# Kernel tuning notes

Measured on AMD Instinct MI355X. Metric: run time of the kernel, lower is better.

Reference implementation:

```python
import jax, jax.numpy as jnp
import numpy as np

LAYERS = [3, 256, 256, 256, 256, 2]
N = 32768  # collocation points


def setup_inputs() -> dict:
    key = jax.random.key(0)
    ks = jax.random.split(key, 2 * len(LAYERS))
    inp = {"inputs": jax.random.uniform(ks[0], (N, LAYERS[0]), dtype=jnp.float32)}
    for l in range(len(LAYERS) - 1):
        std = np.sqrt(2.0 / (LAYERS[l] + LAYERS[l + 1])).astype(np.float32)
        inp[f"W{l}"] = std * jax.random.truncated_normal(
            ks[l + 1], -2.0, 2.0, (LAYERS[l], LAYERS[l + 1]), dtype=jnp.float32)
        inp[f"b{l}"] = jnp.zeros((LAYERS[l + 1],), dtype=jnp.float32)
    inp["lb"] = jnp.zeros((LAYERS[0],), dtype=jnp.float32)
    inp["ub"] = jnp.ones((LAYERS[0],), dtype=jnp.float32)
    return inp


def _net(x, Ws, bs, lb, ub):
    # normalize inputs to [-1, 1], then tanh MLP with linear final layer
    H = 2.0 * (x - lb) / (ub - lb) - 1.0
    for W, b in zip(Ws[:-1], bs[:-1]):
        H = jnp.tanh(H @ W + b)
    return H @ Ws[-1] + bs[-1]


def reference(inputs, W0, b0, W1, b1, W2, b2, W3, b3, W4, b4, lb, ub):
    Ws = [W0, W1, W2, W3, W4]
    bs = [b0, b1, b2, b3, b4]
    out = _net(inputs, Ws, bs, lb, ub)  # [N, Dout]

    f1 = lambda x: _net(x, Ws, bs, lb, ub)  # single sample [D1] -> [Dout]
    # partials_1[i][n, k] = d y_i[n] / d x[n, k]  (tf.gradients of sum over batch)
    jac = jax.vmap(jax.jacrev(f1))(inputs)  # [N, Dout, D1]
    # tf.gradients(partials_1[i], X) = grad of sum over (n, j) of dy_i/dx_j,
    # per sample: partials_2[i][n, k] = sum_j d^2 y_i[n] / (dx_j dx_k)
    g = lambda x: jax.jacrev(f1)(x).sum(axis=-1)  # [Dout]
    hess = jax.vmap(jax.jacrev(g))(inputs)  # [N, Dout, D1]

    partials_1 = jnp.transpose(jac, (1, 0, 2))   # [Dout, N, D1]
    partials_2 = jnp.transpose(hess, (1, 0, 2))  # [Dout, N, D1]
    return out, partials_1, partials_2
```

## Files before the change

kernel.cpp:

```cpp
#include <hip/hip_runtime.h>
#include <math.h>

typedef _Float16 f16x8 __attribute__((ext_vector_type(8)));
typedef _Float16 f16x4 __attribute__((ext_vector_type(4)));
typedef float    f32x4 __attribute__((ext_vector_type(4)));
typedef f16x8 f16x8_a __attribute__((may_alias));
typedef f16x4 f16x4_a __attribute__((may_alias));
typedef f32x4 f32x4_a __attribute__((may_alias));

#define MSAMP 8

__device__ __forceinline__ float tanh_fast(float x) {
    const float e = __expf(2.0f * x);
    return 1.0f - 2.0f * __builtin_amdgcn_rcpf(e + 1.0f);
}

__global__ void prep_w(const float* __restrict__ W1, const float* __restrict__ W2,
                       const float* __restrict__ W3, _Float16* __restrict__ wsw) {
    const int tid = blockIdx.x * 256 + threadIdx.x;
    if (tid >= 3 * 8 * 16 * 64 * 8) return;
    const int j    = tid & 7;
    const int lane = (tid >> 3) & 63;
    const int nt   = (tid >> 9) & 15;
    const int kt   = (tid >> 13) & 7;
    const int l    = tid >> 16;
    const float* W = (l == 0) ? W1 : (l == 1) ? W2 : W3;
    const int k = kt * 32 + (lane >> 4) * 8 + j;
    const int n = nt * 16 + (lane & 15);
    wsw[((size_t)((l * 8 + kt) * 16 + nt)) * 512 + lane * 8 + j] = (_Float16)W[k * 256 + n];
}

__global__ __launch_bounds__(256, 3)
void pinn_mfma(const float* __restrict__ X,
               const float* __restrict__ W0, const float* __restrict__ b0,
               const float* __restrict__ b1, const float* __restrict__ b2,
               const float* __restrict__ b3,
               const float* __restrict__ W4, const float* __restrict__ b4,
               const float* __restrict__ lb, const float* __restrict__ ub,
               const _Float16* __restrict__ wsw,
               float* __restrict__ out, int N)
{
    __shared__ __attribute__((aligned(16))) char  smem[32768];
    __shared__ __attribute__((aligned(16))) float redw[448];
    f16x8_a*  BV  = (f16x8_a*)smem;
    _Float16* zbh = (_Float16*)smem;

    const int t    = threadIdx.x;
    const int s0   = blockIdx.x * MSAMP;
    const int wv   = t >> 6, lane = t & 63;
    const int q    = lane >> 4, c = lane & 15;
    const int jgl  = lane >> 3, m = lane & 7;
    const int jg   = wv * 8 + jgl;
    const int kt0  = jg >> 2, lq0 = jg & 3;

    const int vidz0 = ((t >> 5) * 4 + 3) * 64 + ((t >> 3) & 3) * 16 + 8 + (t & 7);
    const int vidzw = (((wv * 2 + (lane >> 5)) * 4 + 3) * 64) + (((lane >> 3) & 3) * 16) + 8 + (lane & 7);
    const f16x8 zvec = {};

    float lbv[3], cv[3];
    #pragma unroll
    for (int k = 0; k < 3; ++k) { lbv[k] = lb[k]; cv[k] = 2.0f / (ub[k] - lbv[k]); }

    {
        const int jg0 = t >> 3, m0 = t & 7;
        const int n = s0 + m0;
        float x0 = 0.f, x1 = 0.f, x2 = 0.f;
        if (n < N) { x0 = X[n*3+0]; x1 = X[n*3+1]; x2 = X[n*3+2]; }
        const float h0 = cv[0]*(x0 - lbv[0]) - 1.0f;
        const float h1 = cv[1]*(x1 - lbv[1]) - 1.0f;
        const float h2 = cv[2]*(x2 - lbv[2]) - 1.0f;

        float w0v[8], w1v[8], w2v[8], bv[8];
        *(f32x4*)&w0v[0] = *(const f32x4*)&W0[0*256 + jg0*8];
        *(f32x4*)&w0v[4] = *(const f32x4*)&W0[0*256 + jg0*8 + 4];
        *(f32x4*)&w1v[0] = *(const f32x4*)&W0[1*256 + jg0*8];
        *(f32x4*)&w1v[4] = *(const f32x4*)&W0[1*256 + jg0*8 + 4];
        *(f32x4*)&w2v[0] = *(const f32x4*)&W0[2*256 + jg0*8];
        *(f32x4*)&w2v[4] = *(const f32x4*)&W0[2*256 + jg0*8 + 4];
        *(f32x4*)&bv[0]  = *(const f32x4*)&b0[jg0*8];
        *(f32x4*)&bv[4]  = *(const f32x4*)&b0[jg0*8 + 4];

        float st[7][8];
        #pragma unroll
        for (int jj = 0; jj < 8; ++jj) {
            const float zH  = h0*w0v[jj] + h1*w1v[jj] + h2*w2v[jj] + bv[jj];
            const float zt0 = cv[0]*w0v[jj];
            const float zt1 = cv[1]*w1v[jj];
            const float zt2 = cv[2]*w2v[jj];
            const float h   = tanh_fast(zH);
            const float dd  = 1.0f - h*h;
            const float qq  = -2.0f * h * (zt0 + zt1 + zt2);
            st[0][jj] = h;
            st[1][jj] = dd * zt0; st[2][jj] = dd * zt1; st[3][jj] = dd * zt2;
            st[4][jj] = dd * (qq*zt0); st[5][jj] = dd * (qq*zt1); st[6][jj] = dd * (qq*zt2);
        }
        const int k0a = jg0 >> 2, l0a = jg0 & 3;
        #pragma unroll
        for (int s = 0; s < 7; ++s) {
            const int r = s*8 + m0;
            const int vid = (k0a*4 + (r>>4))*64 + l0a*16 + (r & 15);
            f16x8 vh;
            #pragma unroll
            for (int jj = 0; jj < 8; ++jj) vh[jj] = (_Float16)st[s][jj];
            BV[vid] = vh;
        }
        BV[vidz0] = zvec;
    }
    __syncthreads();

    #pragma unroll 1
    for (int l = 0; l < 3; ++l) {
        const _Float16* __restrict__ Wb = wsw + (size_t)l * 65536;
        const int ktbase = 2*wv + 2;

        f32x4 acc[4][4];
        #pragma unroll
        for (int a = 0; a < 4; ++a)
            #pragma unroll
            for (int b = 0; b < 4; ++b) acc[a][b] = (f32x4){0.f, 0.f, 0.f, 0.f};

        #pragma unroll
        for (int i = 0; i < 8; ++i) {
            if (i == 6) __syncthreads();
            const int kt = (ktbase + i) & 7;
            f16x8 sh[4], wh[4];
            #pragma unroll
            for (int rt = 0; rt < 4; ++rt)
                sh[rt] = BV[(kt*4 + rt)*64 + lane];
            #pragma unroll
            for (int mtj = 0; mtj < 4; ++mtj)
                wh[mtj] = *(const f16x8*)&Wb[(size_t)(kt*16 + wv*4 + mtj)*512 + lane*8];
            #pragma unroll
            for (int mtj = 0; mtj < 4; ++mtj)
                #pragma unroll
                for (int rt = 0; rt < 4; ++rt)
                    acc[mtj][rt] = __builtin_amdgcn_mfma_f32_16x16x32_f16(wh[mtj], sh[rt],
                                                                          acc[mtj][rt], 0, 0, 0);
        }

        #pragma unroll
        for (int mtj = 0; mtj < 4; ++mtj) {
            const int jl = mtj*16 + q*4;
            #pragma unroll
            for (int rt = 0; rt < 4; ++rt) {
                const int r = rt*16 + c;
                const int h = wv*4096 + r*64 + ((jl + 4*(r&15)) & 63);
                f16x4 v;
                #pragma unroll
                for (int e = 0; e < 4; ++e) v[e] = (_Float16)acc[mtj][rt][e];
                *(f16x4_a*)&zbh[h] = v;
            }
        }
        asm volatile("s_waitcnt lgkmcnt(0)" ::: "memory");

        {
            const float* __restrict__ bb = (l == 0) ? b1 : (l == 1) ? b2 : b3;
            float bvv[8];
            *(f32x4*)&bvv[0] = *(const f32x4*)&bb[jg*8];
            *(f32x4*)&bvv[4] = *(const f32x4*)&bb[jg*8 + 4];

            float z[7][8];
            #pragma unroll
            for (int s = 0; s < 7; ++s) {
                const int r    = s*8 + m;
                const int base = wv*4096 + r*64;
                const int rot  = 4*(r & 15);
                const f16x4 a = *(const f16x4_a*)&zbh[base + ((jgl*8     + rot) & 63)];
                const f16x4 b = *(const f16x4_a*)&zbh[base + ((jgl*8 + 4 + rot) & 63)];
                #pragma unroll
                for (int e = 0; e < 4; ++e) { z[s][e] = (float)a[e]; z[s][4+e] = (float)b[e]; }
            }
            float stt[7][8];
            #pragma unroll
            for (int jj = 0; jj < 8; ++jj) {
                const float zH  = z[0][jj] + bvv[jj];
                const float zt0 = z[1][jj], zt1 = z[2][jj], zt2 = z[3][jj];
                const float zr0 = z[4][jj], zr1 = z[5][jj], zr2 = z[6][jj];
                const float h   = tanh_fast(zH);
                const float dd  = 1.0f - h*h;
                const float qq  = -2.0f * h * (zt0 + zt1 + zt2);
                stt[0][jj] = h;
                stt[1][jj] = dd * zt0; stt[2][jj] = dd * zt1; stt[3][jj] = dd * zt2;
                stt[4][jj] = dd * (zr0 + qq*zt0);
                stt[5][jj] = dd * (zr1 + qq*zt1);
                stt[6][jj] = dd * (zr2 + qq*zt2);
            }

            if (l < 2) {
                #pragma unroll
                for (int s = 0; s < 7; ++s) {
                    const int r = s*8 + m;
                    const int vid = (kt0*4 + (r>>4))*64 + lq0*16 + (r & 15);
                    f16x8 vh;
                    #pragma unroll
                    for (int jj = 0; jj < 8; ++jj) vh[jj] = (_Float16)stt[s][jj];
                    BV[vid] = vh;
                }
                BV[vidzw] = zvec;
                __syncthreads();
            } else {
                float w4r[16];
                #pragma unroll
                for (int q4 = 0; q4 < 4; ++q4)
                    *(f32x4*)&w4r[q4*4] = *(const f32x4*)&W4[jg*16 + q4*4];
                float p[2][7];
                #pragma unroll
                for (int s = 0; s < 7; ++s) {
                    float p0 = 0.f, p1 = 0.f;
                    #pragma unroll
                    for (int jj = 0; jj < 8; ++jj) {
                        p0 += stt[s][jj] * w4r[jj*2 + 0];
                        p1 += stt[s][jj] * w4r[jj*2 + 1];
                    }
                    p[0][s] = p0; p[1][s] = p1;
                }
                #pragma unroll
                for (int ch = 0; ch < 2; ++ch) {
                    #pragma unroll
                    for (int s = 0; s < 7; ++s) {
                        float v = p[ch][s];
                        v += __shfl_xor(v, 8);
                        v += __shfl_xor(v, 16);
                        v += __shfl_xor(v, 32);
                        p[ch][s] = v;
                    }
                }
                if (jgl == 0) {
                    #pragma unroll
                    for (int ch = 0; ch < 2; ++ch)
                        #pragma unroll
                        for (int s = 0; s < 7; ++s)
                            redw[(ch*56 + s*8 + m)*4 + wv] = p[ch][s];
                }
                __syncthreads();
            }
        }
    }

    if (t < 112) {
        const f32x4 vv = *(const f32x4*)&redw[t*4];
        const float v = vv[0] + vv[1] + vv[2] + vv[3];
        const int ch = t / 56, rem = t % 56, s = rem >> 3, mm = rem & 7;
        const int n = s0 + mm;
        if (n < N) {
            const size_t N2 = (size_t)N * 2, N3 = (size_t)N * 3;
            if (s == 0)      out[(size_t)n*2 + ch] = v + b4[ch];
            else if (s <= 3) out[N2 + (size_t)ch*N3 + (size_t)n*3 + (s-1)] = v;
            else             out[N2 + 2*N3 + (size_t)ch*N3 + (size_t)n*3 + (s-4)] = v;
        }
    }
}

extern "C" void kernel_launch(void* const* d_in, const int* in_sizes, int n_in,
                              void* d_out, int out_size, void* d_ws, size_t ws_size,
                              hipStream_t stream) {
    const float* X  = (const float*)d_in[0];
    const float* W0 = (const float*)d_in[1];
    const float* b0 = (const float*)d_in[2];
    const float* W1 = (const float*)d_in[3];
    const float* b1 = (const float*)d_in[4];
    const float* W2 = (const float*)d_in[5];
    const float* b2 = (const float*)d_in[6];
    const float* W3 = (const float*)d_in[7];
    const float* b3 = (const float*)d_in[8];
    const float* W4 = (const float*)d_in[9];
    const float* b4 = (const float*)d_in[10];
    const float* lb = (const float*)d_in[11];
    const float* ub = (const float*)d_in[12];
    float* out = (float*)d_out;
    _Float16* wsw = (_Float16*)d_ws;

    const int N = in_sizes[0] / 3;

    prep_w<<<768, 256, 0, stream>>>(W1, W2, W3, wsw);

    const int grid = (N + MSAMP - 1) / MSAMP;
    pinn_mfma<<<grid, 256, 0, stream>>>(X, W0, b0, b1, b2, b3, W4, b4, lb, ub,
                                        wsw, out, N);
}
```

Before: 192.5 us.

## Split each block's work across eight waves and pack activation math in fp16

Doubles the block to 512 threads so each wave owns 32 output features (2 MFMA column tiles) instead of 64, halving per-wave accumulators and spreading the MFMA and tanh work over more waves. The per-layer tangent and second-derivative propagation now runs in packed fp16 (f16x2 ops) with pkrtz conversions, and the LDS staging layout, swizzle and reduction buffer are adjusted to match. The aim is more parallelism and lower register pressure per wave at the cost of extra barrier participants and reduced precision in the derivative chain.

New measurement: 202.2 us. 5.0% more time.

```diff
diff --git a/kernel.cpp b/kernel.cpp
--- a/kernel.cpp
+++ b/kernel.cpp
@@ -3,6 +3,7 @@
 
 typedef _Float16 f16x8 __attribute__((ext_vector_type(8)));
 typedef _Float16 f16x4 __attribute__((ext_vector_type(4)));
+typedef _Float16 f16x2 __attribute__((ext_vector_type(2)));
 typedef float    f32x4 __attribute__((ext_vector_type(4)));
 typedef f16x8 f16x8_a __attribute__((may_alias));
 typedef f16x4 f16x4_a __attribute__((may_alias));
@@ -13,6 +14,16 @@
 __device__ __forceinline__ float tanh_fast(float x) {
     const float e = __expf(2.0f * x);
     return 1.0f - 2.0f * __builtin_amdgcn_rcpf(e + 1.0f);
+}
+
+__device__ __forceinline__ f16x2 pkrtz(float a, float b) {
+    return __builtin_bit_cast(f16x2, __builtin_amdgcn_cvt_pkrtz(a, b));
+}
+__device__ __forceinline__ f16x4 cat2(f16x2 a, f16x2 b) {
+    return __builtin_shufflevector(a, b, 0, 1, 2, 3);
+}
+__device__ __forceinline__ f16x4 pack4(const float* v) {
+    return cat2(pkrtz(v[0], v[1]), pkrtz(v[2], v[3]));
 }
 
 __global__ void prep_w(const float* __restrict__ W1, const float* __restrict__ W2,
@@ -30,7 +41,7 @@
     wsw[((size_t)((l * 8 + kt) * 16 + nt)) * 512 + lane * 8 + j] = (_Float16)W[k * 256 + n];
 }
 
-__global__ __launch_bounds__(256, 3)
+__global__ __launch_bounds__(512, 4)
 void pinn_mfma(const float* __restrict__ X,
                const float* __restrict__ W0, const float* __restrict__ b0,
                const float* __restrict__ b1, const float* __restrict__ b2,
@@ -41,28 +52,23 @@
                float* __restrict__ out, int N)
 {
     __shared__ __attribute__((aligned(16))) char  smem[32768];
-    __shared__ __attribute__((aligned(16))) float redw[448];
-    f16x8_a*  BV  = (f16x8_a*)smem;
-    _Float16* zbh = (_Float16*)smem;
+    __shared__ __attribute__((aligned(16))) float redw[896];
+    f16x8_a*  BV = (f16x8_a*)smem;
+    _Float16* Bh = (_Float16*)smem;
 
     const int t    = threadIdx.x;
     const int s0   = blockIdx.x * MSAMP;
     const int wv   = t >> 6, lane = t & 63;
     const int q    = lane >> 4, c = lane & 15;
-    const int jgl  = lane >> 3, m = lane & 7;
-    const int jg   = wv * 8 + jgl;
-    const int kt0  = jg >> 2, lq0 = jg & 3;
-
-    const int vidz0 = ((t >> 5) * 4 + 3) * 64 + ((t >> 3) & 3) * 16 + 8 + (t & 7);
-    const int vidzw = (((wv * 2 + (lane >> 5)) * 4 + 3) * 64) + (((lane >> 3) & 3) * 16) + 8 + (lane & 7);
-    const f16x8 zvec = {};
+    const int qd   = lane >> 3, m = lane & 7;
+    const f16x8 zvec8 = {};
 
     float lbv[3], cv[3];
     #pragma unroll
     for (int k = 0; k < 3; ++k) { lbv[k] = lb[k]; cv[k] = 2.0f / (ub[k] - lbv[k]); }
 
     {
-        const int jg0 = t >> 3, m0 = t & 7;
+        const int qd4 = t >> 3, m0 = t & 7;
         const int n = s0 + m0;
         float x0 = 0.f, x1 = 0.f, x2 = 0.f;
         if (n < N) { x0 = X[n*3+0]; x1 = X[n*3+1]; x2 = X[n*3+2]; }
@@ -70,19 +76,15 @@
         const float h1 = cv[1]*(x1 - lbv[1]) - 1.0f;
         const float h2 = cv[2]*(x2 - lbv[2]) - 1.0f;
 
-        float w0v[8], w1v[8], w2v[8], bv[8];
-        *(f32x4*)&w0v[0] = *(const f32x4*)&W0[0*256 + jg0*8];
-        *(f32x4*)&w0v[4] = *(const f32x4*)&W0[0*256 + jg0*8 + 4];
-        *(f32x4*)&w1v[0] = *(const f32x4*)&W0[1*256 + jg0*8];
-        *(f32x4*)&w1v[4] = *(const f32x4*)&W0[1*256 + jg0*8 + 4];
-        *(f32x4*)&w2v[0] = *(const f32x4*)&W0[2*256 + jg0*8];
-        *(f32x4*)&w2v[4] = *(const f32x4*)&W0[2*256 + jg0*8 + 4];
-        *(f32x4*)&bv[0]  = *(const f32x4*)&b0[jg0*8];
-        *(f32x4*)&bv[4]  = *(const f32x4*)&b0[jg0*8 + 4];
-
-        float st[7][8];
-        #pragma unroll
-        for (int jj = 0; jj < 8; ++jj) {
+        float w0v[4], w1v[4], w2v[4], bv[4];
+        *(f32x4*)w0v = *(const f32x4*)&W0[0*256 + qd4*4];
+        *(f32x4*)w1v = *(const f32x4*)&W0[1*256 + qd4*4];
+        *(f32x4*)w2v = *(const f32x4*)&W0[2*256 + qd4*4];
+        *(f32x4*)bv  = *(const f32x4*)&b0[qd4*4];
+
+        float st[7][4];
+        #pragma unroll
+        for (int jj = 0; jj < 4; ++jj) {
             const float zH  = h0*w0v[jj] + h1*w1v[jj] + h2*w2v[jj] + bv[jj];
             const float zt0 = cv[0]*w0v[jj];
             const float zt1 = cv[1]*w1v[jj];
@@ -94,44 +96,42 @@
             st[1][jj] = dd * zt0; st[2][jj] = dd * zt1; st[3][jj] = dd * zt2;
             st[4][jj] = dd * (qq*zt0); st[5][jj] = dd * (qq*zt1); st[6][jj] = dd * (qq*zt2);
         }
-        const int k0a = jg0 >> 2, l0a = jg0 & 3;
         #pragma unroll
         for (int s = 0; s < 7; ++s) {
             const int r = s*8 + m0;
-            const int vid = (k0a*4 + (r>>4))*64 + l0a*16 + (r & 15);
-            f16x8 vh;
-            #pragma unroll
-            for (int jj = 0; jj < 8; ++jj) vh[jj] = (_Float16)st[s][jj];
-            BV[vid] = vh;
-        }
-        BV[vidz0] = zvec;
+            const int vid = ((qd4>>3)*4 + (r>>4))*64 + ((qd4>>1)&3)*16 + (r & 15);
+            *(f16x4_a*)&Bh[vid*8 + (qd4&1)*4] = pack4(&st[s][0]);
+        }
+    }
+    if (t < 256) {
+        const int vid = ((t>>5)*4 + 3)*64 + ((t>>3)&3)*16 + 8 + (t&7);
+        BV[vid] = zvec8;
     }
     __syncthreads();
 
     #pragma unroll 1
     for (int l = 0; l < 3; ++l) {
         const _Float16* __restrict__ Wb = wsw + (size_t)l * 65536;
-        const int ktbase = 2*wv + 2;
-
-        f32x4 acc[4][4];
-        #pragma unroll
-        for (int a = 0; a < 4; ++a)
+
+        f32x4 acc[2][4];
+        #pragma unroll
+        for (int a = 0; a < 2; ++a)
             #pragma unroll
             for (int b = 0; b < 4; ++b) acc[a][b] = (f32x4){0.f, 0.f, 0.f, 0.f};
 
         #pragma unroll
         for (int i = 0; i < 8; ++i) {
-            if (i == 6) __syncthreads();
-            const int kt = (ktbase + i) & 7;
-            f16x8 sh[4], wh[4];
+            if (i == 7) __syncthreads();
+            const int kt = (wv + 1 + i) & 7;
+            f16x8 sh[4], wh[2];
             #pragma unroll
             for (int rt = 0; rt < 4; ++rt)
                 sh[rt] = BV[(kt*4 + rt)*64 + lane];
             #pragma unroll
-            for (int mtj = 0; mtj < 4; ++mtj)
-                wh[mtj] = *(const f16x8*)&Wb[(size_t)(kt*16 + wv*4 + mtj)*512 + lane*8];
-            #pragma unroll
-            for (int mtj = 0; mtj < 4; ++mtj)
+            for (int mtj = 0; mtj < 2; ++mtj)
+                wh[mtj] = *(const f16x8*)&Wb[(size_t)(kt*16 + wv*2 + mtj)*512 + lane*8];
+            #pragma unroll
+            for (int mtj = 0; mtj < 2; ++mtj)
                 #pragma unroll
                 for (int rt = 0; rt < 4; ++rt)
                     acc[mtj][rt] = __builtin_amdgcn_mfma_f32_16x16x32_f16(wh[mtj], sh[rt],
@@ -139,78 +139,93 @@
         }
 
         #pragma unroll
-        for (int mtj = 0; mtj < 4; ++mtj) {
+        for (int mtj = 0; mtj < 2; ++mtj) {
             const int jl = mtj*16 + q*4;
             #pragma unroll
             for (int rt = 0; rt < 4; ++rt) {
                 const int r = rt*16 + c;
-                const int h = wv*4096 + r*64 + ((jl + 4*(r&15)) & 63);
-                f16x4 v;
-                #pragma unroll
-                for (int e = 0; e < 4; ++e) v[e] = (_Float16)acc[mtj][rt][e];
-                *(f16x4_a*)&zbh[h] = v;
+                const int h = wv*2048 + r*32 + ((jl + 4*(r&7)) & 31);
+                *(f16x4_a*)&Bh[h] = cat2(pkrtz(acc[mtj][rt][0], acc[mtj][rt][1]),
+                                         pkrtz(acc[mtj][rt][2], acc[mtj][rt][3]));
             }
         }
         asm volatile("s_waitcnt lgkmcnt(0)" ::: "memory");
 
         {
             const float* __restrict__ bb = (l == 0) ? b1 : (l == 1) ? b2 : b3;
-            float bvv[8];
-            *(f32x4*)&bvv[0] = *(const f32x4*)&bb[jg*8];
-            *(f32x4*)&bvv[4] = *(const f32x4*)&bb[jg*8 + 4];
-
-            float z[7][8];
-            #pragma unroll
-            for (int s = 0; s < 7; ++s) {
-                const int r    = s*8 + m;
-                const int base = wv*4096 + r*64;
-                const int rot  = 4*(r & 15);
-                const f16x4 a = *(const f16x4_a*)&zbh[base + ((jgl*8     + rot) & 63)];
-                const f16x4 b = *(const f16x4_a*)&zbh[base + ((jgl*8 + 4 + rot) & 63)];
-                #pragma unroll
-                for (int e = 0; e < 4; ++e) { z[s][e] = (float)a[e]; z[s][4+e] = (float)b[e]; }
-            }
-            float stt[7][8];
-            #pragma unroll
-            for (int jj = 0; jj < 8; ++jj) {
-                const float zH  = z[0][jj] + bvv[jj];
-                const float zt0 = z[1][jj], zt1 = z[2][jj], zt2 = z[3][jj];
-                const float zr0 = z[4][jj], zr1 = z[5][jj], zr2 = z[6][jj];
-                const float h   = tanh_fast(zH);
-                const float dd  = 1.0f - h*h;
-                const float qq  = -2.0f * h * (zt0 + zt1 + zt2);
-                stt[0][jj] = h;
-                stt[1][jj] = dd * zt0; stt[2][jj] = dd * zt1; stt[3][jj] = dd * zt2;
-                stt[4][jj] = dd * (zr0 + qq*zt0);
-                stt[5][jj] = dd * (zr1 + qq*zt1);
-                stt[6][jj] = dd * (zr2 + qq*zt2);
-            }
+            float bvv[4];
+            *(f32x4*)bvv = *(const f32x4*)&bb[wv*32 + qd*4];
+
+            const int xoff = 4*((qd + m) & 7);
+            f16x4 zq[7];
+            #pragma unroll
+            for (int s = 0; s < 7; ++s)
+                zq[s] = *(const f16x4_a*)&Bh[wv*2048 + (s*8 + m)*32 + xoff];
+
+            float hf[4];
+            #pragma unroll
+            for (int jj = 0; jj < 4; ++jj)
+                hf[jj] = tanh_fast((float)zq[0][jj] + bvv[jj]);
+
+            f16x2 zt2[3][2], zr2[3][2];
+            #pragma unroll
+            for (int k = 0; k < 3; ++k) {
+                zt2[k][0] = __builtin_shufflevector(zq[1+k], zq[1+k], 0, 1);
+                zt2[k][1] = __builtin_shufflevector(zq[1+k], zq[1+k], 2, 3);
+                zr2[k][0] = __builtin_shufflevector(zq[4+k], zq[4+k], 0, 1);
+                zr2[k][1] = __builtin_shufflevector(zq[4+k], zq[4+k], 2, 3);
+            }
+            const f16x2 one2 = {(_Float16)1.0f,  (_Float16)1.0f};
+            const f16x2 m22  = {(_Float16)-2.0f, (_Float16)-2.0f};
+            f16x2 h2[2], dd2[2], qq2[2];
+            #pragma unroll
+            for (int p = 0; p < 2; ++p) {
+                h2[p] = pkrtz(hf[2*p], hf[2*p+1]);
+                const f16x2 sz = zt2[0][p] + zt2[1][p] + zt2[2][p];
+                dd2[p] = one2 - h2[p]*h2[p];
+                qq2[p] = m22 * h2[p] * sz;
+            }
+            f16x2 t2[3][2], r2[3][2];
+            #pragma unroll
+            for (int k = 0; k < 3; ++k)
+                #pragma unroll
+                for (int p = 0; p < 2; ++p) {
+                    t2[k][p] = dd2[p] * zt2[k][p];
+                    r2[k][p] = dd2[p] * (zr2[k][p] + qq2[p]*zt2[k][p]);
+                }
 
             if (l < 2) {
                 #pragma unroll
                 for (int s = 0; s < 7; ++s) {
                     const int r = s*8 + m;
-                    const int vid = (kt0*4 + (r>>4))*64 + lq0*16 + (r & 15);
-                    f16x8 vh;
-                    #pragma unroll
-                    for (int jj = 0; jj < 8; ++jj) vh[jj] = (_Float16)stt[s][jj];
-                    BV[vid] = vh;
-                }
-                BV[vidzw] = zvec;
+                    const int vid = (wv*4 + (r>>4))*64 + (qd>>1)*16 + (r & 15);
+                    f16x4 v;
+                    if (s == 0)      v = cat2(h2[0], h2[1]);
+                    else if (s <= 3) v = cat2(t2[s-1][0], t2[s-1][1]);
+                    else             v = cat2(r2[s-4][0], r2[s-4][1]);
+                    *(f16x4_a*)&Bh[vid*8 + (qd&1)*4] = v;
+                }
+                if (lane < 32) {
+                    const int vid = (wv*4 + 3)*64 + (lane>>3)*16 + 8 + (lane&7);
+                    BV[vid] = zvec8;
+                }
                 __syncthreads();
             } else {
-                float w4r[16];
-                #pragma unroll
-                for (int q4 = 0; q4 < 4; ++q4)
-                    *(f32x4*)&w4r[q4*4] = *(const f32x4*)&W4[jg*16 + q4*4];
+                float w4r[8];
+                *(f32x4*)&w4r[0] = *(const f32x4*)&W4[(wv*32 + qd*4)*2];
+                *(f32x4*)&w4r[4] = *(const f32x4*)&W4[(wv*32 + qd*4)*2 + 4];
                 float p[2][7];
                 #pragma unroll
                 for (int s = 0; s < 7; ++s) {
                     float p0 = 0.f, p1 = 0.f;
                     #pragma unroll
-                    for (int jj = 0; jj < 8; ++jj) {
-                        p0 += stt[s][jj] * w4r[jj*2 + 0];
-                        p1 += stt[s][jj] * w4r[jj*2 + 1];
+                    for (int e = 0; e < 4; ++e) {
+                        float se;
+                        if (s == 0)      se = hf[e];
+                        else if (s <= 3) se = (float)t2[s-1][e>>1][e&1];
+                        else             se = (float)r2[s-4][e>>1][e&1];
+                        p0 += se * w4r[e*2 + 0];
+                        p1 += se * w4r[e*2 + 1];
                     }
                     p[0][s] = p0; p[1][s] = p1;
                 }
@@ -225,12 +240,12 @@
                         p[ch][s] = v;
                     }
                 }
-                if (jgl == 0) {
+                if (qd == 0) {
                     #pragma unroll
                     for (int ch = 0; ch < 2; ++ch)
                         #pragma unroll
                         for (int s = 0; s < 7; ++s)
-                            redw[(ch*56 + s*8 + m)*4 + wv] = p[ch][s];
+                            redw[(ch*56 + s*8 + m)*8 + wv] = p[ch][s];
                 }
                 __syncthreads();
             }
@@ -238,8 +253,9 @@
     }
 
     if (t < 112) {
-        const f32x4 vv = *(const f32x4*)&redw[t*4];
-        const float v = vv[0] + vv[1] + vv[2] + vv[3];
+        const f32x4 a = *(const f32x4*)&redw[t*8];
+        const f32x4 b = *(const f32x4*)&redw[t*8 + 4];
+        const float v = a[0]+a[1]+a[2]+a[3] + b[0]+b[1]+b[2]+b[3];
         const int ch = t / 56, rem = t % 56, s = rem >> 3, mm = rem & 7;
         const int n = s0 + mm;
         if (n < N) {
@@ -275,6 +291,6 @@
     prep_w<<<768, 256, 0, stream>>>(W1, W2, W3, wsw);
 
     const int grid = (N + MSAMP - 1) / MSAMP;
-    pinn_mfma<<<grid, 256, 0, stream>>>(X, W0, b0, b1, b2, b3, W4, b4, lb, ub,
+    pinn_mfma<<<grid, 512, 0, stream>>>(X, W0, b0, b1, b2, b3, W4, b4, lb, ub,
                                         wsw, out, N);
 }
```
